# Kernel optimization log

Hardware: AMD Instinct MI355X
Metric: run time of the kernel (lower is better)

Reference implementation:

```python
import jax, jax.numpy as jnp
import numpy as np

BATCH, SEQ, DMODEL, DHID = 4, 4096, 1024, 1024
R_MIN, R_MAX = 0.9, 0.99
MAX_PHASE = np.pi / 50  # module overrides ctor arg with pi/50
EPS = 1e-5


def setup_inputs() -> dict:
    key = jax.random.key(0)
    ks = jax.random.split(key, 8)
    # nu_init
    u1 = jax.random.uniform(ks[0], (DHID,)) * (1 - EPS) + EPS
    mag_sq = u1 * (R_MAX ** 2 - R_MIN ** 2) + R_MIN ** 2
    nu_log = jnp.log(-0.5 * jnp.log(mag_sq + EPS))
    # theta_init
    u2 = jax.random.uniform(ks[1], (DHID,)) * (1 - EPS) + EPS
    theta_log = jnp.log(MAX_PHASE * u2)
    B_re = jax.random.normal(ks[2], (DHID, DMODEL)) / np.sqrt(2 * DMODEL)
    B_im = jax.random.normal(ks[3], (DHID, DMODEL)) / np.sqrt(2 * DMODEL)
    C_re = jax.random.normal(ks[4], (DMODEL, DHID)) / np.sqrt(DHID)
    C_im = jax.random.normal(ks[5], (DMODEL, DHID)) / np.sqrt(DHID)
    D_skip = jax.random.normal(ks[6], (DMODEL,))
    inputs = jax.random.normal(ks[7], (BATCH, SEQ, DMODEL), dtype=jnp.float32)
    return {"inputs": inputs, "nu_log": nu_log, "theta_log": theta_log,
            "B_re": B_re, "B_im": B_im, "C_re": C_re, "C_im": C_im,
            "D_skip": D_skip}


def reference(inputs, nu_log, theta_log, B_re, B_im, C_re, C_im, D_skip):
    nu = jnp.exp(nu_log)
    theta = jnp.exp(theta_log)
    diag_lambda = jnp.exp(-nu + 1j * theta)            # [H] complex
    # forward recomputes gamma_log from nu_log (parameter gamma_log unused)
    gamma_log = 0.5 * jnp.log(1 - jnp.exp(-2 * jnp.exp(nu_log)) + EPS)
    B_norm = (B_re + 1j * B_im) * jnp.exp(gamma_log)[:, None]  # [H, D]
    inputs_c = inputs.astype(jnp.complex64)
    Bu = jnp.einsum('hd,btd->bth', B_norm, inputs_c)   # [B, T, H]

    def step(h, bu_t):
        h = diag_lambda * h + bu_t
        return h, h

    h0 = jnp.zeros((inputs.shape[0], diag_lambda.shape[0]), dtype=Bu.dtype)
    _, hs = jax.lax.scan(step, h0, jnp.swapaxes(Bu, 0, 1))  # [T, B, H]
    hs = jnp.swapaxes(hs, 0, 1)                              # [B, T, H]
    C_complex = C_re + 1j * C_im                              # [D, H]
    out = jnp.einsum('bth,dh->btd', hs, C_complex).real + inputs * D_skip
    return out.astype(jnp.float32)
```

## Files before the change

### kernel.cpp

```cpp
#include <hip/hip_runtime.h>


typedef __bf16 bf16x8 __attribute__((ext_vector_type(8)));
typedef float floatx4 __attribute__((ext_vector_type(4)));

__device__ __forceinline__ unsigned short f2bf(float f) {
  unsigned u = __float_as_uint(f);
  u += 0x7fffu + ((u >> 16) & 1u);
  return (unsigned short)(u >> 16);
}
__device__ __forceinline__ float bf2f(unsigned short s) {
  return __uint_as_float(((unsigned)s) << 16);
}


__global__ void prep_params(const float* __restrict__ nu_log,
                            const float* __restrict__ theta_log,
                            float* __restrict__ lam,
                            float* __restrict__ lamL,
                            float* __restrict__ gamma)
{
  int h = blockIdx.x * 256 + threadIdx.x;
  float nu = expf(nu_log[h]);
  float th = expf(theta_log[h]);
  float r = expf(-nu);
  lam[h]        = r * cosf(th);
  lam[1024 + h] = r * sinf(th);
  float rL = expf(-128.0f * nu);
  lamL[h]        = rL * cosf(128.0f * th);
  lamL[1024 + h] = rL * sinf(128.0f * th);
  gamma[h] = sqrtf(1.0f - expf(-2.0f * nu) + 1e-5f);
}

__global__ void prep_B(const float* __restrict__ B_re, const float* __restrict__ B_im,
                       const float* __restrict__ gamma, unsigned short* __restrict__ Bcat)
{
  int tid = blockIdx.x * 256 + threadIdx.x;
  int n = tid >> 10;
  int d = tid & 1023;
  int h = n & 1023;
  float v = (n < 1024 ? B_re[h * 1024 + d] : B_im[h * 1024 + d]) * gamma[h];
  Bcat[tid] = f2bf(v);
}

__global__ void prep_C(const float* __restrict__ C_re, const float* __restrict__ C_im,
                       unsigned short* __restrict__ Ccat)
{
  int tid = blockIdx.x * 256 + threadIdx.x;
  int d = tid >> 11;
  int k = tid & 2047;
  float v = (k < 1024) ? C_re[d * 1024 + k] : -C_im[d * 1024 + (k - 1024)];
  Ccat[tid] = f2bf(v);
}

__global__ void conv_inputs(const float* __restrict__ in, unsigned short* __restrict__ outb)
{
  int tid = blockIdx.x * 256 + threadIdx.x;
  float4 v = ((const float4*)in)[tid];
  unsigned lo = (unsigned)f2bf(v.x) | ((unsigned)f2bf(v.y) << 16);
  unsigned hi = (unsigned)f2bf(v.z) | ((unsigned)f2bf(v.w) << 16);
  ((uint2*)outb)[tid] = make_uint2(lo, hi);
}


#define GLDS(gp, lp) __builtin_amdgcn_global_load_lds(                        \
      (const __attribute__((address_space(1))) void*)(gp),                    \
      (__attribute__((address_space(3))) void*)(lp), 16, 0, 0)

#define STAGE(kt, buf) do {                                                   \
    const int _ko = (kt) * 32;                                                \
    GLDS(gA0 + _ko, &As[(buf)][lofs0]);                                       \
    GLDS(gA1 + _ko, &As[(buf)][lofs1]);                                       \
    GLDS(gB0 + _ko, &Bs[(buf)][lofs0]);                                       \
    GLDS(gB1 + _ko, &Bs[(buf)][lofs1]);                                       \
  } while (0)

#define GLDS_A(kt) do {                                                       \
    const int _ko = (kt) * 32;  const int _b = (kt) & 3;                      \
    GLDS(gA0 + _ko, &As[_b][lofs0]);                                          \
    GLDS(gA1 + _ko, &As[_b][lofs1]);                                          \
  } while (0)

#define GLDS_B(kt) do {                                                       \
    const int _ko = (kt) * 32;  const int _b = (kt) & 3;                      \
    GLDS(gB0 + _ko, &Bs[_b][lofs0]);                                          \
    GLDS(gB1 + _ko, &Bs[_b][lofs1]);                                          \
  } while (0)

#define RD_B(buf) do {                                                        \
    _Pragma("unroll")                                                         \
    for (int j = 0; j < 4; ++j) {                                             \
      const int r = wn * 64 + j * 16 + lm;                                    \
      bfr[j] = *reinterpret_cast<const bf16x8*>(                              \
          &Bs[(buf)][r * 32 + (q ^ ((r >> 1) & 3)) * 8]);                     \
    }                                                                         \
  } while (0)

#define RD_A(buf, i0) do {                                                    \
    _Pragma("unroll")                                                         \
    for (int i = 0; i < 4; ++i) {                                             \
      const int r = wm * 128 + ((i0) + i) * 16 + lm;                          \
      afr[(i0) + i] = *reinterpret_cast<const bf16x8*>(                       \
          &As[(buf)][r * 32 + (q ^ ((r >> 1) & 3)) * 8]);                     \
    }                                                                         \
  } while (0)

#define MFMA16(i0) do {                                                       \
    __builtin_amdgcn_s_setprio(1);                                            \
    _Pragma("unroll")                                                         \
    for (int i = 0; i < 4; ++i)                                               \
      _Pragma("unroll")                                                       \
      for (int j = 0; j < 4; ++j)                                             \
        acc[(i0) + i][j] = __builtin_amdgcn_mfma_f32_16x16x32_bf16(           \
            afr[(i0) + i], bfr[j], acc[(i0) + i][j], 0, 0, 0);                \
    __builtin_amdgcn_s_setprio(0);                                            \
  } while (0)

#define SB0() __builtin_amdgcn_sched_barrier(0)

#define VMW(n) do {                                                           \
    SB0();                                                                    \
    asm volatile("s_waitcnt vmcnt(" #n ")" ::: "memory");                     \
    SB0();                                                                    \
  } while (0)

#define BAR() do {                                                            \
    SB0();                                                                    \
    asm volatile("" ::: "memory");                                            \
    __builtin_amdgcn_s_barrier();                                             \
    asm volatile("" ::: "memory");                                            \
    SB0();                                                                    \
  } while (0)

#define LGKM0() do {                                                          \
    asm volatile("s_waitcnt lgkmcnt(0)" ::: "memory");                        \
    SB0();                                                                    \
  } while (0)

#define BODY(kt_) do {                                                        \
    const int _cur = (kt_) & 3;                                               \
                                                                 \
    RD_B(_cur);                                                               \
    RD_A(_cur, 0);                                                            \
    GLDS_A((kt_) + 3);                                                        \
    BAR();                                                                    \
    LGKM0();                                                                  \
    MFMA16(0);                                                                \
                                                                 \
    RD_A(_cur, 4);                                                            \
    GLDS_B((kt_) + 3);                                                        \
    VMW(8);                                                                   \
    BAR();                                                                    \
    LGKM0();                                                                  \
    MFMA16(4);                                                                \
  } while (0)

#define TAIL(kt_, vm_) do {                                                   \
    const int _cur = (kt_) & 3;                                               \
    RD_B(_cur);                                                               \
    RD_A(_cur, 0);                                                            \
    BAR();                                                                    \
    LGKM0();                                                                  \
    MFMA16(0);                                                                \
    RD_A(_cur, 4);                                                            \
    VMW(vm_);                                                                 \
    BAR();                                                                    \
    LGKM0();                                                                  \
    MFMA16(4);                                                                \
  } while (0)

template <int EPI>
__global__ __launch_bounds__(512, 2) void gemm256_kernel(
    const unsigned short* __restrict__ A,
    const unsigned short* __restrict__ Bt,
    void* __restrict__ Cout,
    int M, int N, int K,
    const float* __restrict__ skip_in,
    const float* __restrict__ skip_w)
{
  __shared__ __align__(16) unsigned short As[4][256 * 32];
  __shared__ __align__(16) unsigned short Bs[4][256 * 32];

  const int tid  = threadIdx.x;
  const int lane = tid & 63;
  const int wave = tid >> 6;
  const int wm = wave >> 2;
  const int wn = wave & 3;

  const int flat    = blockIdx.x;
  const int xcd     = flat & 7;
  const int local   = flat >> 3;
  const int m_tile  = xcd * 8 + (local & 7);
  const int n_tile  = local >> 3;
  const int m0 = m_tile * 256;
  const int n0 = n_tile * 256;

  const int ldr = lane >> 2;
  const int pos = lane & 3;
  const int lm  = lane & 15;
  const int q   = lane >> 4;

  const int r0 = wave * 32 + ldr;
  const int r1 = r0 + 16;
  const int ca0 = pos ^ ((r0 >> 1) & 3);
  const int ca1 = pos ^ ((r1 >> 1) & 3);

  const unsigned short* gA0 = A  + (size_t)(m0 + r0) * K + ca0 * 8;
  const unsigned short* gA1 = A  + (size_t)(m0 + r1) * K + ca1 * 8;
  const unsigned short* gB0 = Bt + (size_t)(n0 + r0) * K + ca0 * 8;
  const unsigned short* gB1 = Bt + (size_t)(n0 + r1) * K + ca1 * 8;
  const int lofs0 = r0 * 32 + pos * 8;
  const int lofs1 = r1 * 32 + pos * 8;

  floatx4 acc[8][4];
#pragma unroll
  for (int i = 0; i < 8; ++i)
#pragma unroll
    for (int j = 0; j < 4; ++j)
      acc[i][j] = (floatx4){0.f, 0.f, 0.f, 0.f};

  const int KT = K >> 5;

  bf16x8 afr[8], bfr[4];

  STAGE(0, 0);
  STAGE(1, 1);
  STAGE(2, 2);
  VMW(8);
  BAR();

  for (int kt = 0; kt + 3 < KT; ++kt)
    BODY(kt);

  TAIL(KT - 3, 4);
  TAIL(KT - 2, 0);
  {
    const int _cur = (KT - 1) & 3;
    RD_B(_cur);
    RD_A(_cur, 0);
    LGKM0();
    MFMA16(0);
    RD_A(_cur, 4);
    LGKM0();
    MFMA16(4);
  }

#pragma unroll
  for (int i = 0; i < 8; ++i) {
#pragma unroll
    for (int j = 0; j < 4; ++j) {
      const int row0 = m0 + wm * 128 + i * 16 + q * 4;
      const int col  = n0 + wn * 64 + j * 16 + lm;
#pragma unroll
      for (int r = 0; r < 4; ++r) {
        const size_t idx = (size_t)(row0 + r) * N + col;
        if (EPI == 0) {
          ((unsigned short*)Cout)[idx] = f2bf(acc[i][j][r]);
        } else {
          ((float*)Cout)[idx] = acc[i][j][r] + skip_in[idx] * skip_w[col];
        }
      }
    }
  }
}


__global__ void scan_finals(const unsigned short* __restrict__ Bu,
                            const float* __restrict__ lam,
                            float2* __restrict__ finals)
{
  int tid = blockIdx.x * 256 + threadIdx.x;
  int h = tid & 1023, c = (tid >> 10) & 31, b = tid >> 15;
  float lre = lam[h], lim = lam[1024 + h];
  const unsigned short* p = Bu + ((size_t)(b * 4096 + c * 128) * 2048) + h;
  float yre = 0.f, yim = 0.f;
#pragma unroll 4
  for (int t = 0; t < 128; ++t) {
    float ure = bf2f(p[0]);
    float uim = bf2f(p[1024]);
    float nre = fmaf(lre, yre, fmaf(-lim, yim, ure));
    float nim = fmaf(lre, yim, fmaf(lim, yre, uim));
    yre = nre; yim = nim;
    p += 2048;
  }
  finals[tid] = make_float2(yre, yim);
}

__global__ void scan_carries(const float2* __restrict__ finals,
                             const float* __restrict__ lamL,
                             float2* __restrict__ carry)
{
  int tid = blockIdx.x * 256 + threadIdx.x;
  int h = tid & 1023, b = tid >> 10;
  float Lre = lamL[h], Lim = lamL[1024 + h];
  float Hre = 0.f, Him = 0.f;
  for (int c = 0; c < 32; ++c) {
    size_t i = ((size_t)(b * 32 + c) << 10) + h;
    carry[i] = make_float2(Hre, Him);
    float2 f = finals[i];
    float nre = fmaf(Lre, Hre, fmaf(-Lim, Him, f.x));
    float nim = fmaf(Lre, Him, fmaf(Lim, Hre, f.y));
    Hre = nre; Him = nim;
  }
}

__global__ void scan_apply(const float* __restrict__ lam,
                           const float2* __restrict__ carry,
                           unsigned short* __restrict__ Bu)
{
  int tid = blockIdx.x * 256 + threadIdx.x;
  int h = tid & 1023, c = (tid >> 10) & 31, b = tid >> 15;
  float lre = lam[h], lim = lam[1024 + h];
  float2 cv = carry[tid];
  float yre = cv.x, yim = cv.y;
  unsigned short* p = Bu + ((size_t)(b * 4096 + c * 128) * 2048) + h;
#pragma unroll 4
  for (int t = 0; t < 128; ++t) {
    float ure = bf2f(p[0]);
    float uim = bf2f(p[1024]);
    float nre = fmaf(lre, yre, fmaf(-lim, yim, ure));
    float nim = fmaf(lre, yim, fmaf(lim, yre, uim));
    yre = nre; yim = nim;
    p[0]    = f2bf(yre);
    p[1024] = f2bf(yim);
    p += 2048;
  }
}


extern "C" void kernel_launch(void* const* d_in, const int* in_sizes, int n_in,
                              void* d_out, int out_size, void* d_ws, size_t ws_size,
                              hipStream_t stream)
{
  const float* inputs    = (const float*)d_in[0];
  const float* nu_log    = (const float*)d_in[1];
  const float* theta_log = (const float*)d_in[2];
  const float* B_re      = (const float*)d_in[3];
  const float* B_im      = (const float*)d_in[4];
  const float* C_re      = (const float*)d_in[5];
  const float* C_im      = (const float*)d_in[6];
  const float* D_skip    = (const float*)d_in[7];
  float* out = (float*)d_out;

  char* ws = (char*)d_ws;
  float* lam   = (float*)ws;
  float* lamL  = lam + 2048;
  float* gamma = lamL + 2048;
  unsigned short* inp_bf = (unsigned short*)(ws + (1 << 16));
  unsigned short* Bcat   = inp_bf + (size_t)16384 * 1024;
  unsigned short* Ccat   = Bcat   + (size_t)2048 * 1024;
  unsigned short* Bu     = Ccat   + (size_t)1024 * 2048;
  float2* finals = (float2*)(Bu + (size_t)16384 * 2048);
  float2* carry  = finals + 131072;

  prep_params<<<4,    256, 0, stream>>>(nu_log, theta_log, lam, lamL, gamma);
  prep_B     <<<8192, 256, 0, stream>>>(B_re, B_im, gamma, Bcat);
  prep_C     <<<8192, 256, 0, stream>>>(C_re, C_im, Ccat);
  conv_inputs<<<16384,256, 0, stream>>>(inputs, inp_bf);

  gemm256_kernel<0><<<512, 512, 0, stream>>>(
      inp_bf, Bcat, Bu, 16384, 2048, 1024, nullptr, nullptr);

  scan_finals <<<512, 256, 0, stream>>>(Bu, lam, finals);
  scan_carries<<<16,  256, 0, stream>>>(finals, lamL, carry);
  scan_apply  <<<512, 256, 0, stream>>>(lam, carry, Bu);

  gemm256_kernel<1><<<256, 512, 0, stream>>>(
      Bu, Ccat, out, 16384, 1024, 2048, inputs, D_skip);
}
```

Before: 327.7 us.

## Software-pipeline LDS fragment reads across k-iterations with one barrier per step

Restructures the GEMM main loop so the B and first-half A fragments for the next k-tile are read from LDS at the end of the current iteration. Partial lgkmcnt waits let the first MFMA block start while the second half of A is still loading. This cuts barriers from two per k-step to one and overlaps LDS latency with MFMA work. The cost is more live fragment registers and tighter vmcnt accounting, which could be wrong if the counts do not match the staged loads.

```diff
diff --git a/kernel.cpp b/kernel.cpp
--- a/kernel.cpp
+++ b/kernel.cpp
@@ -124,6 +124,12 @@
     SB0();                                                                    \
   } while (0)
 
+#define LGKMC(n) do {                                                         \
+    SB0();                                                                    \
+    asm volatile("s_waitcnt lgkmcnt(" #n ")" ::: "memory");                   \
+    SB0();                                                                    \
+  } while (0)
+
 #define BAR() do {                                                            \
     SB0();                                                                    \
     asm volatile("" ::: "memory");                                            \
@@ -132,41 +138,34 @@
     SB0();                                                                    \
   } while (0)
 
-#define LGKM0() do {                                                          \
-    asm volatile("s_waitcnt lgkmcnt(0)" ::: "memory");                        \
-    SB0();                                                                    \
-  } while (0)
-
-#define BODY(kt_) do {                                                        \
+#define BODY_FULL(kt_) do {                                                   \
     const int _cur = (kt_) & 3;                                               \
-                                                                 \
-    RD_B(_cur);                                                               \
-    RD_A(_cur, 0);                                                            \
+    const int _nxt = ((kt_) + 1) & 3;                                         \
+    RD_A(_cur, 4);                    \
     GLDS_A((kt_) + 3);                                                        \
+    LGKMC(4);                                 \
+    MFMA16(0);                                \
+    LGKMC(0);                            \
+    MFMA16(4);                                \
+    RD_B(_nxt);                              \
+    RD_A(_nxt, 0);                                                            \
+    GLDS_B((kt_) + 3);                                                        \
+    VMW(4);                                            \
     BAR();                                                                    \
-    LGKM0();                                                                  \
+  } while (0)
+
+#define BODY_NOSTAGE(kt_, vm_) do {                                           \
+    const int _cur = (kt_) & 3;                                               \
+    const int _nxt = ((kt_) + 1) & 3;                                         \
+    RD_A(_cur, 4);                                                            \
+    LGKMC(4);                                                                 \
     MFMA16(0);                                                                \
-                                                                 \
-    RD_A(_cur, 4);                                                            \
-    GLDS_B((kt_) + 3);                                                        \
-    VMW(8);                                                                   \
-    BAR();                                                                    \
-    LGKM0();                                                                  \
+    LGKMC(0);                                                                 \
     MFMA16(4);                                                                \
-  } while (0)
-
-#define TAIL(kt_, vm_) do {                                                   \
-    const int _cur = (kt_) & 3;                                               \
-    RD_B(_cur);                                                               \
-    RD_A(_cur, 0);                                                            \
-    BAR();                                                                    \
-    LGKM0();                                                                  \
-    MFMA16(0);                                                                \
-    RD_A(_cur, 4);                                                            \
+    RD_B(_nxt);                                                               \
+    RD_A(_nxt, 0);                                                            \
     VMW(vm_);                                                                 \
     BAR();                                                                    \
-    LGKM0();                                                                  \
-    MFMA16(4);                                                                \
   } while (0)
 
 template <int EPI>
@@ -226,22 +225,22 @@
   STAGE(0, 0);
   STAGE(1, 1);
   STAGE(2, 2);
-  VMW(8);
+  VMW(4);
   BAR();
+  RD_B(0);
+  RD_A(0, 0);
 
   for (int kt = 0; kt + 3 < KT; ++kt)
-    BODY(kt);
-
-  TAIL(KT - 3, 4);
-  TAIL(KT - 2, 0);
+    BODY_FULL(kt);
+
+  BODY_NOSTAGE(KT - 3, 0);
+  BODY_NOSTAGE(KT - 2, 0);
   {
     const int _cur = (KT - 1) & 3;
-    RD_B(_cur);
-    RD_A(_cur, 0);
-    LGKM0();
+    RD_A(_cur, 4);
+    LGKMC(4);
     MFMA16(0);
-    RD_A(_cur, 4);
-    LGKM0();
+    LGKMC(0);
     MFMA16(4);
   }
 
```

Result: faster. 319.6 us (-2.5%).
